# Kernel tuning notes

Measured on AMD Instinct MI355X. Metric: run time of the kernel, lower is better.

Reference implementation:

```python
import jax, jax.numpy as jnp
import numpy as np

RETURN_SHAPE = (128, 128)


def dht2(x):
    # Discrete Hartley Transform over the spatial axes (2, 3):
    # H = Re(FFT) - Im(FFT). Unnormalized, matching scipy.fft default.
    f = jnp.fft.fftn(x, axes=(2, 3))
    return f.real - f.imag


def setup_inputs() -> dict:
    key = jax.random.key(0)
    x = jax.random.normal(key, (8, 64, 256, 256), dtype=jnp.float32)
    return {"x": x}


def reference(x) -> jnp.ndarray:
    # Spectral pooling: DHT -> center crop in frequency domain -> DHT.
    h_out, w_out = RETURN_SHAPE
    H, W = x.shape[2], x.shape[3]
    d = dht2(x)
    sh = (H - h_out) // 2
    sw = (W - w_out) // 2
    cropped = d[:, :, sh:sh + h_out, sw:sw + w_out]
    return dht2(cropped).astype(jnp.float32)
```

## Files before the change

### kernel.cpp

```cpp
#include <hip/hip_runtime.h>
#include <math.h>


typedef __attribute__((ext_vector_type(8))) short bfrag;
typedef __attribute__((ext_vector_type(4))) float ffrag;

#define PI2_256 0.0245436926061702597f
#define PI2_128 0.0490873852123405194f

__device__ __forceinline__ unsigned short f2bf(float f) {
    union { float f; unsigned int u; } v; v.f = f;
    unsigned int r = v.u + 0x7fffu + ((v.u >> 16) & 1u);
    return (unsigned short)(r >> 16);
}

__device__ __forceinline__ bfrag pack8(float4 a, float4 b) {
    bfrag r;
    r[0] = (short)f2bf(a.x); r[1] = (short)f2bf(a.y);
    r[2] = (short)f2bf(a.z); r[3] = (short)f2bf(a.w);
    r[4] = (short)f2bf(b.x); r[5] = (short)f2bf(b.y);
    r[6] = (short)f2bf(b.z); r[7] = (short)f2bf(b.w);
    return r;
}

__device__ __forceinline__ uint2 packlohi(ffrag a) {
    uint2 r;
    r.x = (unsigned int)f2bf(a[0]) | ((unsigned int)f2bf(a[1]) << 16);
    r.y = (unsigned int)f2bf(a[2]) | ((unsigned int)f2bf(a[3]) << 16);
    return r;
}

template<int NCOLS, int K>
__device__ __forceinline__ void stageB(const unsigned short* __restrict__ src,
                                       unsigned short* __restrict__ Lb, int t)
{
    constexpr int CHUNKS = NCOLS * K / 8;
#pragma unroll
    for (int i = 0; i < CHUNKS / 512; ++i) {
        const int o = (t + i * 512) * 8;
        const int j = o / K;
        const int k = o - j * K;
        const uint4 v = *(const uint4*)(src + o);
        *(uint4*)&Lb[j * K + (((k >> 3) ^ (j & 7)) << 3)] = v;
    }
}

template<int K>
__device__ __forceinline__ bfrag ldsB(const unsigned short* __restrict__ Lb, int j, int k)
{
    return *(const bfrag*)&Lb[j * K + (((k >> 3) ^ (j & 7)) << 3)];
}

__global__ __launch_bounds__(256) void gen_tables(unsigned short* __restrict__ ws)
{
    const int id = blockIdx.x * 256 + threadIdx.x;
    {
        const int j = id >> 8, m = id & 255;
        const int mult = (j < 128) ? (64 + j) : (320 - j);
        const int idx = (mult * m) & 255;
        float s, c; sincosf((float)idx * PI2_256, &s, &c);
        ws[id] = f2bf(c + s);
    }
    {
        const int u = id >> 9, k = id & 511;
        const int up = 64 + u;
        float s, c, val;
        if (k < 256) { sincosf((float)((up * k) & 255) * PI2_256, &s, &c); val = c; }
        else         { sincosf((float)((up * (k - 256)) & 255) * PI2_256, &s, &c); val = s; }
        ws[65536 + id] = f2bf(val);
    }
    if (id < 32768) {
        {
            const int j = id >> 7, m = id & 127;
            const int mult = (j < 128) ? j : (256 - j);
            const int idx = (mult * m) & 127;
            float s, c; sincosf((float)idx * PI2_128, &s, &c);
            ws[131072 + id] = f2bf(c + s);
        }
        {
            const int u = id >> 8, k = id & 255;
            float s, c, val;
            if (k < 128) { sincosf((float)((u * k) & 127) * PI2_128, &s, &c); val = c; }
            else         { sincosf((float)((u * (k - 128)) & 127) * PI2_128, &s, &c); val = s; }
            ws[163840 + id] = f2bf(val);
        }
    }
}

__global__ __launch_bounds__(512, 2) void pass1(const float* __restrict__ X,
                                                const unsigned short* __restrict__ ws,
                                                unsigned short* __restrict__ Ct)
{
    __shared__ unsigned short Lb[256 * 256];

    const int t  = threadIdx.x;
    const int w  = t >> 6;
    const int ln = t & 15;
    const int q  = (t & 63) >> 4;

    stageB<256, 256>(ws, Lb, t);
    __syncthreads();

    const int img = blockIdx.x >> 1;
    const int nb  = (blockIdx.x & 1) * 128;
    const float* __restrict__ Ar = X + (size_t)img * 65536 + (size_t)(nb + 16 * w + ln) * 256;

    ffrag acc[16];
#pragma unroll
    for (int nt = 0; nt < 16; ++nt) acc[nt] = (ffrag){0.f, 0.f, 0.f, 0.f};

    for (int kk = 0; kk < 8; ++kk) {
        const int k = kk * 32 + q * 8;
        const float4 x0 = *(const float4*)(Ar + k);
        const float4 x1 = *(const float4*)(Ar + k + 4);
        const bfrag A = pack8(x0, x1);
#pragma unroll
        for (int nt = 0; nt < 16; ++nt) {
            const bfrag B = ldsB<256>(Lb, nt * 16 + ln, k);
            acc[nt] = __builtin_amdgcn_mfma_f32_16x16x32_bf16(A, B, acc[nt], 0, 0, 0);
        }
    }
    unsigned short* __restrict__ Co = Ct + (size_t)img * 65536 + nb + 16 * w + 4 * q;
#pragma unroll
    for (int nt = 0; nt < 16; ++nt) {
        *(uint2*)&Co[(size_t)(nt * 16 + ln) * 256] = packlohi(acc[nt]);
    }
}

__global__ __launch_bounds__(512, 2) void pass2(const unsigned short* __restrict__ Ct,
                                                const unsigned short* __restrict__ ws,
                                                unsigned short* __restrict__ Dc)
{
    __shared__ unsigned short Lb[128 * 512];

    const int t  = threadIdx.x;
    const int w  = t >> 6;
    const int ln = t & 15;
    const int q  = (t & 63) >> 4;

    stageB<128, 512>(ws + 65536, Lb, t);
    __syncthreads();

    const int img = blockIdx.x;
    const unsigned short* __restrict__ Abase = Ct + (size_t)img * 65536;
    const int v = 16 * w + ln;

    ffrag acc[8];
#pragma unroll
    for (int nt = 0; nt < 8; ++nt) acc[nt] = (ffrag){0.f, 0.f, 0.f, 0.f};

#pragma unroll
    for (int kh = 0; kh < 2; ++kh) {
        const unsigned short* __restrict__ Ar = Abase + (size_t)(v + kh * 128) * 256;
        for (int kk = 0; kk < 8; ++kk) {
            const int k = kk * 32 + q * 8;
            const bfrag A = *(const bfrag*)(Ar + k);
            const int kfull = kh * 256 + k;
#pragma unroll
            for (int nt = 0; nt < 8; ++nt) {
                const bfrag B = ldsB<512>(Lb, nt * 16 + ln, kfull);
                acc[nt] = __builtin_amdgcn_mfma_f32_16x16x32_bf16(A, B, acc[nt], 0, 0, 0);
            }
        }
    }
    unsigned short* __restrict__ Do = Dc + (size_t)img * 16384 + 16 * w + 4 * q;
#pragma unroll
    for (int nt = 0; nt < 8; ++nt) {
        *(uint2*)&Do[(size_t)(nt * 16 + ln) * 128] = packlohi(acc[nt]);
    }
}

__global__ __launch_bounds__(512, 2) void pass3(const unsigned short* __restrict__ Dc,
                                                const unsigned short* __restrict__ ws,
                                                unsigned short* __restrict__ C3t)
{
    __shared__ unsigned short Lb[256 * 128];

    const int t  = threadIdx.x;
    const int w  = t >> 6;
    const int ln = t & 15;
    const int q  = (t & 63) >> 4;

    stageB<256, 128>(ws + 131072, Lb, t);
    __syncthreads();

    const int img = blockIdx.x;
    const unsigned short* __restrict__ Ar = Dc + (size_t)img * 16384 + (size_t)(16 * w + ln) * 128;

    ffrag acc[16];
#pragma unroll
    for (int nt = 0; nt < 16; ++nt) acc[nt] = (ffrag){0.f, 0.f, 0.f, 0.f};

    for (int kk = 0; kk < 4; ++kk) {
        const int k = kk * 32 + q * 8;
        const bfrag A = *(const bfrag*)(Ar + k);
#pragma unroll
        for (int nt = 0; nt < 16; ++nt) {
            const bfrag B = ldsB<128>(Lb, nt * 16 + ln, k);
            acc[nt] = __builtin_amdgcn_mfma_f32_16x16x32_bf16(A, B, acc[nt], 0, 0, 0);
        }
    }
    unsigned short* __restrict__ Co = C3t + (size_t)img * 32768 + 16 * w + 4 * q;
#pragma unroll
    for (int nt = 0; nt < 16; ++nt) {
        *(uint2*)&Co[(size_t)(nt * 16 + ln) * 128] = packlohi(acc[nt]);
    }
}

__global__ __launch_bounds__(512, 2) void pass4(const unsigned short* __restrict__ C3t,
                                                const unsigned short* __restrict__ ws,
                                                float* __restrict__ out)
{
    __shared__ unsigned short Lb[128 * 256];

    const int t  = threadIdx.x;
    const int w  = t >> 6;
    const int ln = t & 15;
    const int q  = (t & 63) >> 4;

    stageB<128, 256>(ws + 163840, Lb, t);
    __syncthreads();

    const int img = blockIdx.x;
    const unsigned short* __restrict__ Abase = C3t + (size_t)img * 32768;
    const int v = 16 * w + ln;

    ffrag acc[8];
#pragma unroll
    for (int nt = 0; nt < 8; ++nt) acc[nt] = (ffrag){0.f, 0.f, 0.f, 0.f};

#pragma unroll
    for (int kh = 0; kh < 2; ++kh) {
        const unsigned short* __restrict__ Ar = Abase + (size_t)(v + kh * 128) * 128;
        for (int kk = 0; kk < 4; ++kk) {
            const int k = kk * 32 + q * 8;
            const bfrag A = *(const bfrag*)(Ar + k);
            const int kfull = kh * 128 + k;
#pragma unroll
            for (int nt = 0; nt < 8; ++nt) {
                const bfrag B = ldsB<256>(Lb, nt * 16 + ln, kfull);
                acc[nt] = __builtin_amdgcn_mfma_f32_16x16x32_bf16(A, B, acc[nt], 0, 0, 0);
            }
        }
    }
    float* __restrict__ G = out + (size_t)img * 16384 + 16 * w + 4 * q;
#pragma unroll
    for (int nt = 0; nt < 8; ++nt) {
        float4 o4 = make_float4(acc[nt][0], acc[nt][1], acc[nt][2], acc[nt][3]);
        *(float4*)&G[(size_t)(nt * 16 + ln) * 128] = o4;
    }
}

__global__ __launch_bounds__(512, 2) void stage1_old(const float* __restrict__ X,
                                                     const unsigned short* __restrict__ ws,
                                                     float* __restrict__ dc)
{
    __shared__ unsigned short PQt[128 * 512];

    const int t  = threadIdx.x;
    const int w  = t >> 6;
    const int ln = t & 15;
    const int q  = (t & 63) >> 4;
    const int img = blockIdx.x;

    const float* __restrict__ Xi = X + (size_t)img * 65536;
    const unsigned short* __restrict__ W1 = ws;
    const unsigned short* __restrict__ W2 = ws + 65536;

    {
        ffrag acc[2][16];
#pragma unroll
        for (int mt = 0; mt < 2; ++mt)
#pragma unroll
            for (int nt = 0; nt < 16; ++nt)
                acc[mt][nt] = (ffrag){0.f, 0.f, 0.f, 0.f};

        const int rowA0 = 32 * w;
        for (int kk = 0; kk < 8; ++kk) {
            const int k = kk * 32 + q * 8;
            bfrag A[2];
#pragma unroll
            for (int mt = 0; mt < 2; ++mt) {
                const float* xp = Xi + (size_t)(rowA0 + 16 * mt + ln) * 256 + k;
                const float4 x0 = *(const float4*)xp;
                const float4 x1 = *(const float4*)(xp + 4);
                A[mt] = pack8(x0, x1);
            }
#pragma unroll
            for (int nt = 0; nt < 16; ++nt) {
                const int j = nt * 16 + ln;
                const bfrag B = *(const bfrag*)(W1 + j * 256 + k);
#pragma unroll
                for (int mt = 0; mt < 2; ++mt)
                    acc[mt][nt] = __builtin_amdgcn_mfma_f32_16x16x32_bf16(A[mt], B, acc[mt][nt], 0, 0, 0);
            }
        }
#pragma unroll
        for (int mt = 0; mt < 2; ++mt) {
#pragma unroll
            for (int nt = 0; nt < 16; ++nt) {
                const int c  = nt * 16 + ln;
                const int v  = c & 127;
                const int kb = ((c < 128) ? 0 : 256) + rowA0 + 16 * mt + 4 * q;
                const uint2 lohi = packlohi(acc[mt][nt]);
                const int phys = v * 512 + (((kb >> 3) ^ (v & 7)) << 3) + (kb & 7);
                *(uint2*)&PQt[phys] = lohi;
            }
        }
    }
    __syncthreads();

    {
        ffrag acc[8];
#pragma unroll
        for (int nt = 0; nt < 8; ++nt) acc[nt] = (ffrag){0.f, 0.f, 0.f, 0.f};

        const int u0 = 16 * w;
        for (int kk = 0; kk < 16; ++kk) {
            const int k = kk * 32 + q * 8;
            const bfrag A = *(const bfrag*)(W2 + (size_t)(u0 + ln) * 512 + k);
#pragma unroll
            for (int nt = 0; nt < 8; ++nt) {
                const int v = nt * 16 + ln;
                const int g = (k >> 3) ^ (v & 7);
                const bfrag B = *(const bfrag*)&PQt[v * 512 + (g << 3)];
                acc[nt] = __builtin_amdgcn_mfma_f32_16x16x32_bf16(A, B, acc[nt], 0, 0, 0);
            }
        }
        float* __restrict__ D = dc + (size_t)img * 16384;
#pragma unroll
        for (int nt = 0; nt < 8; ++nt) {
#pragma unroll
            for (int r = 0; r < 4; ++r) {
                const int u = u0 + 4 * q + r;
                const int v = nt * 16 + ln;
                D[u * 128 + v] = acc[nt][r];
            }
        }
    }
}

__global__ __launch_bounds__(256, 2) void stage2_old(const unsigned short* __restrict__ ws,
                                                     float* __restrict__ io)
{
    __shared__ unsigned short Dcb[128 * 128];
    __shared__ unsigned short PQ2[64 * 256];

    const int t  = threadIdx.x;
    const int w  = t >> 6;
    const int ln = t & 15;
    const int q  = (t & 63) >> 4;
    const int img = blockIdx.x;

    float* __restrict__ G = io + (size_t)img * 16384;
    const unsigned short* __restrict__ W3 = ws + 131072;
    const unsigned short* __restrict__ W4 = ws + 163840;

    {
        const int p = t >> 1, half = t & 1;
        const float* src = G + p * 128 + half * 64;
#pragma unroll
        for (int g = 0; g < 8; ++g) {
            const float4 a = *(const float4*)(src + g * 8);
            const float4 b = *(const float4*)(src + g * 8 + 4);
            const int m0 = half * 64 + g * 8;
            const int gran = (m0 >> 3) ^ (p & 7);
            uint4 val;
            val.x = (unsigned int)f2bf(a.x) | ((unsigned int)f2bf(a.y) << 16);
            val.y = (unsigned int)f2bf(a.z) | ((unsigned int)f2bf(a.w) << 16);
            val.z = (unsigned int)f2bf(b.x) | ((unsigned int)f2bf(b.y) << 16);
            val.w = (unsigned int)f2bf(b.z) | ((unsigned int)f2bf(b.w) << 16);
            *(uint4*)&Dcb[p * 128 + gran * 8] = val;
        }
    }
    __syncthreads();

    for (int vh = 0; vh < 2; ++vh) {
        ffrag acc[2][8];
#pragma unroll
        for (int mt = 0; mt < 2; ++mt)
#pragma unroll
            for (int nt = 0; nt < 8; ++nt)
                acc[mt][nt] = (ffrag){0.f, 0.f, 0.f, 0.f};

        const int p0 = 32 * w;
        for (int kk = 0; kk < 4; ++kk) {
            const int k = kk * 32 + q * 8;
            bfrag A[2];
#pragma unroll
            for (int mt = 0; mt < 2; ++mt) {
                const int p = p0 + 16 * mt + ln;
                const int g = (k >> 3) ^ (p & 7);
                A[mt] = *(const bfrag*)&Dcb[p * 128 + g * 8];
            }
#pragma unroll
            for (int nt = 0; nt < 8; ++nt) {
                const int c = nt * 16 + ln;
                const int j = (c < 64) ? (64 * vh + c) : (128 + 64 * vh + (c - 64));
                const bfrag B = *(const bfrag*)(W3 + j * 128 + k);
#pragma unroll
                for (int mt = 0; mt < 2; ++mt)
                    acc[mt][nt] = __builtin_amdgcn_mfma_f32_16x16x32_bf16(A[mt], B, acc[mt][nt], 0, 0, 0);
            }
        }
        __syncthreads();
#pragma unroll
        for (int mt = 0; mt < 2; ++mt) {
#pragma unroll
            for (int nt = 0; nt < 8; ++nt) {
                const int c  = nt * 16 + ln;
                const int v  = c & 63;
                const int kb = ((c < 64) ? 0 : 128) + p0 + 16 * mt + 4 * q;
                const uint2 lohi = packlohi(acc[mt][nt]);
                const int phys = v * 256 + (((kb >> 3) ^ (v & 7)) << 3) + (kb & 7);
                *(uint2*)&PQ2[phys] = lohi;
            }
        }
        __syncthreads();

        ffrag o[2][4];
#pragma unroll
        for (int mt = 0; mt < 2; ++mt)
#pragma unroll
            for (int nt = 0; nt < 4; ++nt)
                o[mt][nt] = (ffrag){0.f, 0.f, 0.f, 0.f};

        const int u0 = 32 * w;
        for (int kk = 0; kk < 8; ++kk) {
            const int k = kk * 32 + q * 8;
            bfrag A[2];
#pragma unroll
            for (int mt = 0; mt < 2; ++mt)
                A[mt] = *(const bfrag*)(W4 + (size_t)(u0 + 16 * mt + ln) * 256 + k);
#pragma unroll
            for (int nt = 0; nt < 4; ++nt) {
                const int v = nt * 16 + ln;
                const int g = (k >> 3) ^ (v & 7);
                const bfrag B = *(const bfrag*)&PQ2[v * 256 + (g << 3)];
#pragma unroll
                for (int mt = 0; mt < 2; ++mt)
                    o[mt][nt] = __builtin_amdgcn_mfma_f32_16x16x32_bf16(A[mt], B, o[mt][nt], 0, 0, 0);
            }
        }
#pragma unroll
        for (int mt = 0; mt < 2; ++mt) {
#pragma unroll
            for (int nt = 0; nt < 4; ++nt) {
#pragma unroll
                for (int r = 0; r < 4; ++r) {
                    const int u = u0 + 16 * mt + 4 * q + r;
                    const int v = 64 * vh + nt * 16 + ln;
                    G[u * 128 + v] = o[mt][nt][r];
                }
            }
        }
    }
}

extern "C" void kernel_launch(void* const* d_in, const int* in_sizes, int n_in,
                              void* d_out, int out_size, void* d_ws, size_t ws_size,
                              hipStream_t stream)
{
    const float* x = (const float*)d_in[0];
    float* out = (float*)d_out;
    unsigned short* tw = (unsigned short*)d_ws;

    gen_tables<<<dim3(256), dim3(256), 0, stream>>>(tw);

    int G = 512;
    while (G > 1 && (size_t)163840 * (size_t)G + 393216 > ws_size) G >>= 1;

    if ((size_t)163840 * (size_t)G + 393216 <= ws_size) {
        unsigned short* regA  = tw + 196608;
        unsigned short* regDc = regA + (size_t)G * 65536;
        const int nchunks = 512 / G;
        for (int ci = 0; ci < nchunks; ++ci) {
            const float* xc = x + (size_t)ci * G * 65536;
            float* oc = out + (size_t)ci * G * 16384;
            pass1<<<dim3(2 * G), dim3(512), 0, stream>>>(xc, tw, regA);
            pass2<<<dim3(G), dim3(512), 0, stream>>>(regA, tw, regDc);
            pass3<<<dim3(G), dim3(512), 0, stream>>>(regDc, tw, regA);
            pass4<<<dim3(G), dim3(512), 0, stream>>>(regA, tw, oc);
        }
    } else {
        stage1_old<<<dim3(512), dim3(512), 0, stream>>>(x, tw, out);
        stage2_old<<<dim3(512), dim3(256), 0, stream>>>(tw, out);
    }
}
```

Before: 279.1 us.

## Split DHT GEMM passes by output columns and register-block multiple M tiles per wave

Each of the four MFMA passes now splits the twiddle matrix across two blocks by output column half instead of by input rows. Blocks shrink to 256 threads, and each wave computes several 16-row M tiles that share every B fragment read from LDS. The per-block LDS table is halved and LDS traffic per MFMA drops through register reuse. In exchange, pass1 now re-reads the whole fp32 input image in both column-half blocks, doubling that global read traffic, and runs at one block per CU with more accumulator registers.

```diff
diff --git a/kernel.cpp b/kernel.cpp
--- a/kernel.cpp
+++ b/kernel.cpp
@@ -30,14 +30,14 @@
     return r;
 }
 
-template<int NCOLS, int K>
+template<int NCOLS, int K, int NTH>
 __device__ __forceinline__ void stageB(const unsigned short* __restrict__ src,
                                        unsigned short* __restrict__ Lb, int t)
 {
     constexpr int CHUNKS = NCOLS * K / 8;
 #pragma unroll
-    for (int i = 0; i < CHUNKS / 512; ++i) {
-        const int o = (t + i * 512) * 8;
+    for (int i = 0; i < CHUNKS / NTH; ++i) {
+        const int o = (t + i * NTH) * 8;
         const int j = o / K;
         const int k = o - j * K;
         const uint4 v = *(const uint4*)(src + o);
@@ -87,167 +87,222 @@
     }
 }
 
-__global__ __launch_bounds__(512, 2) void pass1(const float* __restrict__ X,
+__global__ __launch_bounds__(256, 1) void pass1(const float* __restrict__ X,
                                                 const unsigned short* __restrict__ ws,
                                                 unsigned short* __restrict__ Ct)
 {
-    __shared__ unsigned short Lb[256 * 256];
+    __shared__ unsigned short Lb[128 * 256];
 
     const int t  = threadIdx.x;
     const int w  = t >> 6;
     const int ln = t & 15;
     const int q  = (t & 63) >> 4;
-
-    stageB<256, 256>(ws, Lb, t);
+    const int img = blockIdx.x >> 1;
+    const int h   = blockIdx.x & 1;
+
+    stageB<128, 256, 256>(ws + h * 32768, Lb, t);
     __syncthreads();
 
-    const int img = blockIdx.x >> 1;
-    const int nb  = (blockIdx.x & 1) * 128;
-    const float* __restrict__ Ar = X + (size_t)img * 65536 + (size_t)(nb + 16 * w + ln) * 256;
-
-    ffrag acc[16];
-#pragma unroll
-    for (int nt = 0; nt < 16; ++nt) acc[nt] = (ffrag){0.f, 0.f, 0.f, 0.f};
-
+    const float* __restrict__ Xi = X + (size_t)img * 65536;
+
+    ffrag acc[4][8];
+#pragma unroll
+    for (int mt = 0; mt < 4; ++mt)
+#pragma unroll
+        for (int nt = 0; nt < 8; ++nt)
+            acc[mt][nt] = (ffrag){0.f, 0.f, 0.f, 0.f};
+
+#pragma unroll
     for (int kk = 0; kk < 8; ++kk) {
         const int k = kk * 32 + q * 8;
-        const float4 x0 = *(const float4*)(Ar + k);
-        const float4 x1 = *(const float4*)(Ar + k + 4);
-        const bfrag A = pack8(x0, x1);
-#pragma unroll
-        for (int nt = 0; nt < 16; ++nt) {
+        bfrag A[4];
+#pragma unroll
+        for (int mt = 0; mt < 4; ++mt) {
+            const float* xp = Xi + (size_t)(64 * w + 16 * mt + ln) * 256 + k;
+            const float4 x0 = *(const float4*)xp;
+            const float4 x1 = *(const float4*)(xp + 4);
+            A[mt] = pack8(x0, x1);
+        }
+#pragma unroll
+        for (int nt = 0; nt < 8; ++nt) {
             const bfrag B = ldsB<256>(Lb, nt * 16 + ln, k);
-            acc[nt] = __builtin_amdgcn_mfma_f32_16x16x32_bf16(A, B, acc[nt], 0, 0, 0);
-        }
-    }
-    unsigned short* __restrict__ Co = Ct + (size_t)img * 65536 + nb + 16 * w + 4 * q;
-#pragma unroll
-    for (int nt = 0; nt < 16; ++nt) {
-        *(uint2*)&Co[(size_t)(nt * 16 + ln) * 256] = packlohi(acc[nt]);
-    }
-}
-
-__global__ __launch_bounds__(512, 2) void pass2(const unsigned short* __restrict__ Ct,
+#pragma unroll
+            for (int mt = 0; mt < 4; ++mt)
+                acc[mt][nt] = __builtin_amdgcn_mfma_f32_16x16x32_bf16(A[mt], B, acc[mt][nt], 0, 0, 0);
+        }
+    }
+#pragma unroll
+    for (int mt = 0; mt < 4; ++mt) {
+        unsigned short* __restrict__ Co = Ct + (size_t)img * 65536 + 64 * w + 16 * mt + 4 * q;
+#pragma unroll
+        for (int nt = 0; nt < 8; ++nt) {
+            *(uint2*)&Co[(size_t)(128 * h + nt * 16 + ln) * 256] = packlohi(acc[mt][nt]);
+        }
+    }
+}
+
+__global__ __launch_bounds__(256, 2) void pass2(const unsigned short* __restrict__ Ct,
                                                 const unsigned short* __restrict__ ws,
                                                 unsigned short* __restrict__ Dc)
 {
-    __shared__ unsigned short Lb[128 * 512];
+    __shared__ unsigned short Lb[64 * 512];
 
     const int t  = threadIdx.x;
     const int w  = t >> 6;
     const int ln = t & 15;
     const int q  = (t & 63) >> 4;
-
-    stageB<128, 512>(ws + 65536, Lb, t);
+    const int img = blockIdx.x >> 1;
+    const int hu  = blockIdx.x & 1;
+
+    stageB<64, 512, 256>(ws + 65536 + hu * 32768, Lb, t);
     __syncthreads();
 
-    const int img = blockIdx.x;
     const unsigned short* __restrict__ Abase = Ct + (size_t)img * 65536;
-    const int v = 16 * w + ln;
-
-    ffrag acc[8];
-#pragma unroll
-    for (int nt = 0; nt < 8; ++nt) acc[nt] = (ffrag){0.f, 0.f, 0.f, 0.f};
+
+    ffrag acc[2][4];
+#pragma unroll
+    for (int mt = 0; mt < 2; ++mt)
+#pragma unroll
+        for (int nt = 0; nt < 4; ++nt)
+            acc[mt][nt] = (ffrag){0.f, 0.f, 0.f, 0.f};
 
 #pragma unroll
     for (int kh = 0; kh < 2; ++kh) {
-        const unsigned short* __restrict__ Ar = Abase + (size_t)(v + kh * 128) * 256;
+#pragma unroll
         for (int kk = 0; kk < 8; ++kk) {
             const int k = kk * 32 + q * 8;
-            const bfrag A = *(const bfrag*)(Ar + k);
             const int kfull = kh * 256 + k;
-#pragma unroll
-            for (int nt = 0; nt < 8; ++nt) {
+            bfrag A[2];
+#pragma unroll
+            for (int mt = 0; mt < 2; ++mt) {
+                const int v = 32 * w + 16 * mt + ln;
+                A[mt] = *(const bfrag*)(Abase + (size_t)(v + kh * 128) * 256 + k);
+            }
+#pragma unroll
+            for (int nt = 0; nt < 4; ++nt) {
                 const bfrag B = ldsB<512>(Lb, nt * 16 + ln, kfull);
-                acc[nt] = __builtin_amdgcn_mfma_f32_16x16x32_bf16(A, B, acc[nt], 0, 0, 0);
-            }
-        }
-    }
-    unsigned short* __restrict__ Do = Dc + (size_t)img * 16384 + 16 * w + 4 * q;
-#pragma unroll
-    for (int nt = 0; nt < 8; ++nt) {
-        *(uint2*)&Do[(size_t)(nt * 16 + ln) * 128] = packlohi(acc[nt]);
-    }
-}
-
-__global__ __launch_bounds__(512, 2) void pass3(const unsigned short* __restrict__ Dc,
+#pragma unroll
+                for (int mt = 0; mt < 2; ++mt)
+                    acc[mt][nt] = __builtin_amdgcn_mfma_f32_16x16x32_bf16(A[mt], B, acc[mt][nt], 0, 0, 0);
+            }
+        }
+    }
+#pragma unroll
+    for (int mt = 0; mt < 2; ++mt) {
+        unsigned short* __restrict__ Do = Dc + (size_t)img * 16384 + 32 * w + 16 * mt + 4 * q;
+#pragma unroll
+        for (int nt = 0; nt < 4; ++nt) {
+            *(uint2*)&Do[(size_t)(64 * hu + nt * 16 + ln) * 128] = packlohi(acc[mt][nt]);
+        }
+    }
+}
+
+__global__ __launch_bounds__(256, 2) void pass3(const unsigned short* __restrict__ Dc,
                                                 const unsigned short* __restrict__ ws,
                                                 unsigned short* __restrict__ C3t)
 {
-    __shared__ unsigned short Lb[256 * 128];
+    __shared__ unsigned short Lb[128 * 128];
 
     const int t  = threadIdx.x;
     const int w  = t >> 6;
     const int ln = t & 15;
     const int q  = (t & 63) >> 4;
-
-    stageB<256, 128>(ws + 131072, Lb, t);
+    const int img = blockIdx.x >> 1;
+    const int hj  = blockIdx.x & 1;
+
+    stageB<128, 128, 256>(ws + 131072 + hj * 16384, Lb, t);
     __syncthreads();
 
-    const int img = blockIdx.x;
-    const unsigned short* __restrict__ Ar = Dc + (size_t)img * 16384 + (size_t)(16 * w + ln) * 128;
-
-    ffrag acc[16];
-#pragma unroll
-    for (int nt = 0; nt < 16; ++nt) acc[nt] = (ffrag){0.f, 0.f, 0.f, 0.f};
-
+    const unsigned short* __restrict__ Abase = Dc + (size_t)img * 16384;
+
+    ffrag acc[2][8];
+#pragma unroll
+    for (int mt = 0; mt < 2; ++mt)
+#pragma unroll
+        for (int nt = 0; nt < 8; ++nt)
+            acc[mt][nt] = (ffrag){0.f, 0.f, 0.f, 0.f};
+
+#pragma unroll
     for (int kk = 0; kk < 4; ++kk) {
         const int k = kk * 32 + q * 8;
-        const bfrag A = *(const bfrag*)(Ar + k);
-#pragma unroll
-        for (int nt = 0; nt < 16; ++nt) {
+        bfrag A[2];
+#pragma unroll
+        for (int mt = 0; mt < 2; ++mt) {
+            const int p = 32 * w + 16 * mt + ln;
+            A[mt] = *(const bfrag*)(Abase + (size_t)p * 128 + k);
+        }
+#pragma unroll
+        for (int nt = 0; nt < 8; ++nt) {
             const bfrag B = ldsB<128>(Lb, nt * 16 + ln, k);
-            acc[nt] = __builtin_amdgcn_mfma_f32_16x16x32_bf16(A, B, acc[nt], 0, 0, 0);
-        }
-    }
-    unsigned short* __restrict__ Co = C3t + (size_t)img * 32768 + 16 * w + 4 * q;
-#pragma unroll
-    for (int nt = 0; nt < 16; ++nt) {
-        *(uint2*)&Co[(size_t)(nt * 16 + ln) * 128] = packlohi(acc[nt]);
-    }
-}
-
-__global__ __launch_bounds__(512, 2) void pass4(const unsigned short* __restrict__ C3t,
+#pragma unroll
+            for (int mt = 0; mt < 2; ++mt)
+                acc[mt][nt] = __builtin_amdgcn_mfma_f32_16x16x32_bf16(A[mt], B, acc[mt][nt], 0, 0, 0);
+        }
+    }
+#pragma unroll
+    for (int mt = 0; mt < 2; ++mt) {
+        unsigned short* __restrict__ Co = C3t + (size_t)img * 32768 + 32 * w + 16 * mt + 4 * q;
+#pragma unroll
+        for (int nt = 0; nt < 8; ++nt) {
+            *(uint2*)&Co[(size_t)(128 * hj + nt * 16 + ln) * 128] = packlohi(acc[mt][nt]);
+        }
+    }
+}
+
+__global__ __launch_bounds__(256, 2) void pass4(const unsigned short* __restrict__ C3t,
                                                 const unsigned short* __restrict__ ws,
                                                 float* __restrict__ out)
 {
-    __shared__ unsigned short Lb[128 * 256];
+    __shared__ unsigned short Lb[64 * 256];
 
     const int t  = threadIdx.x;
     const int w  = t >> 6;
     const int ln = t & 15;
     const int q  = (t & 63) >> 4;
-
-    stageB<128, 256>(ws + 163840, Lb, t);
+    const int img = blockIdx.x >> 1;
+    const int hu  = blockIdx.x & 1;
+
+    stageB<64, 256, 256>(ws + 163840 + hu * 16384, Lb, t);
     __syncthreads();
 
-    const int img = blockIdx.x;
     const unsigned short* __restrict__ Abase = C3t + (size_t)img * 32768;
-    const int v = 16 * w + ln;
-
-    ffrag acc[8];
-#pragma unroll
-    for (int nt = 0; nt < 8; ++nt) acc[nt] = (ffrag){0.f, 0.f, 0.f, 0.f};
+
+    ffrag acc[2][4];
+#pragma unroll
+    for (int mt = 0; mt < 2; ++mt)
+#pragma unroll
+        for (int nt = 0; nt < 4; ++nt)
+            acc[mt][nt] = (ffrag){0.f, 0.f, 0.f, 0.f};
 
 #pragma unroll
     for (int kh = 0; kh < 2; ++kh) {
-        const unsigned short* __restrict__ Ar = Abase + (size_t)(v + kh * 128) * 128;
+#pragma unroll
         for (int kk = 0; kk < 4; ++kk) {
             const int k = kk * 32 + q * 8;
-            const bfrag A = *(const bfrag*)(Ar + k);
             const int kfull = kh * 128 + k;
-#pragma unroll
-            for (int nt = 0; nt < 8; ++nt) {
+            bfrag A[2];
+#pragma unroll
+            for (int mt = 0; mt < 2; ++mt) {
+                const int v = 32 * w + 16 * mt + ln;
+                A[mt] = *(const bfrag*)(Abase + (size_t)(v + kh * 128) * 128 + k);
+            }
+#pragma unroll
+            for (int nt = 0; nt < 4; ++nt) {
                 const bfrag B = ldsB<256>(Lb, nt * 16 + ln, kfull);
-                acc[nt] = __builtin_amdgcn_mfma_f32_16x16x32_bf16(A, B, acc[nt], 0, 0, 0);
-            }
-        }
-    }
-    float* __restrict__ G = out + (size_t)img * 16384 + 16 * w + 4 * q;
-#pragma unroll
-    for (int nt = 0; nt < 8; ++nt) {
-        float4 o4 = make_float4(acc[nt][0], acc[nt][1], acc[nt][2], acc[nt][3]);
-        *(float4*)&G[(size_t)(nt * 16 + ln) * 128] = o4;
+#pragma unroll
+                for (int mt = 0; mt < 2; ++mt)
+                    acc[mt][nt] = __builtin_amdgcn_mfma_f32_16x16x32_bf16(A[mt], B, acc[mt][nt], 0, 0, 0);
+            }
+        }
+    }
+#pragma unroll
+    for (int mt = 0; mt < 2; ++mt) {
+        float* __restrict__ G = out + (size_t)img * 16384 + 32 * w + 16 * mt + 4 * q;
+#pragma unroll
+        for (int nt = 0; nt < 4; ++nt) {
+            float4 o4 = make_float4(acc[mt][nt][0], acc[mt][nt][1], acc[mt][nt][2], acc[mt][nt][3]);
+            *(float4*)&G[(size_t)(64 * hu + nt * 16 + ln) * 128] = o4;
+        }
     }
 }
 
@@ -477,10 +532,10 @@
         for (int ci = 0; ci < nchunks; ++ci) {
             const float* xc = x + (size_t)ci * G * 65536;
             float* oc = out + (size_t)ci * G * 16384;
-            pass1<<<dim3(2 * G), dim3(512), 0, stream>>>(xc, tw, regA);
-            pass2<<<dim3(G), dim3(512), 0, stream>>>(regA, tw, regDc);
-            pass3<<<dim3(G), dim3(512), 0, stream>>>(regDc, tw, regA);
-            pass4<<<dim3(G), dim3(512), 0, stream>>>(regA, tw, oc);
+            pass1<<<dim3(2 * G), dim3(256), 0, stream>>>(xc, tw, regA);
+            pass2<<<dim3(G * 2), dim3(256), 0, stream>>>(regA, tw, regDc);
+            pass3<<<dim3(2 * G), dim3(256), 0, stream>>>(regDc, tw, regA);
+            pass4<<<dim3(2 * G), dim3(256), 0, stream>>>(regA, tw, oc);
         }
     } else {
         stage1_old<<<dim3(512), dim3(512), 0, stream>>>(x, tw, out);
```

Result: slower. 289.1 us (+3.6%).
